# Kernel tuning notes

Measured on AMD Instinct MI355X. Metric: run time of the kernel, lower is better.

Reference implementation:

```python
import jax, jax.numpy as jnp
import numpy as np

BS, NQ, DIM, HEADS, POINTS, LEVELS = 2, 4096, 768, 6, 4, 1
HD = DIM // HEADS
H = W = 64
NV = H * W
EPS = 1e-6


def setup_inputs() -> dict:
    key = jax.random.key(0)
    ks = jax.random.split(key, 16)
    s = 0.02  # param init scale
    return {
        "query": jax.random.normal(ks[0], (BS, NQ, DIM), jnp.float32),
        "reference_points": jax.random.uniform(ks[1], (BS, NQ, LEVELS, 2), jnp.float32),
        "feat": jax.random.normal(ks[2], (BS, NV, DIM), jnp.float32),
        "spatial_shapes": np.array([[H, W]], dtype=np.int64),
        "level_start_index": np.array([0], dtype=np.int64),
        "ln_w": jnp.ones((DIM,), jnp.float32),
        "ln_b": jnp.zeros((DIM,), jnp.float32),
        "vp_w": jax.random.normal(ks[3], (DIM, DIM), jnp.float32) * s,
        "vp_b": jnp.zeros((DIM,), jnp.float32),
        "off_w": jax.random.normal(ks[4], (DIM, HEADS * LEVELS * POINTS * 2), jnp.float32) * s,
        "off_b": jax.random.normal(ks[5], (HEADS * LEVELS * POINTS * 2,), jnp.float32),
        "aw_w": jax.random.normal(ks[6], (DIM, HEADS * LEVELS * POINTS), jnp.float32) * s,
        "aw_b": jnp.zeros((HEADS * LEVELS * POINTS,), jnp.float32),
        "out_w": jax.random.normal(ks[7], (DIM, DIM), jnp.float32) * s,
        "out_b": jnp.zeros((DIM,), jnp.float32),
        "gamma": jax.random.normal(ks[8], (DIM,), jnp.float32) * 0.1,
    }


def _layernorm(x, w, b):
    mu = jnp.mean(x, axis=-1, keepdims=True)
    var = jnp.mean(jnp.square(x - mu), axis=-1, keepdims=True)
    return (x - mu) * jax.lax.rsqrt(var + EPS) * w + b


def _bilinear_sample(img, loc):
    # img: (bs, heads, H, W, hd); loc: (bs, nq, heads, points, 2) in [0,1]
    # matches torch.grid_sample(align_corners=False, padding_mode='zeros')
    bs, heads, h, w, hd = img.shape
    x = loc[..., 0] * w - 0.5
    y = loc[..., 1] * h - 0.5
    x0 = jnp.floor(x)
    y0 = jnp.floor(y)
    wx = x - x0
    wy = y - y0
    x0i = x0.astype(jnp.int32)
    y0i = y0.astype(jnp.int32)
    bi = jnp.arange(bs)[:, None, None, None]
    hi = jnp.arange(heads)[None, None, :, None]

    def gather(yi, xi):
        valid = (xi >= 0) & (xi < w) & (yi >= 0) & (yi < h)
        v = img[bi, hi, jnp.clip(yi, 0, h - 1), jnp.clip(xi, 0, w - 1)]
        return v * valid[..., None].astype(img.dtype)

    v00 = gather(y0i, x0i)
    v01 = gather(y0i, x0i + 1)
    v10 = gather(y0i + 1, x0i)
    v11 = gather(y0i + 1, x0i + 1)
    wx = wx[..., None]
    wy = wy[..., None]
    return (v00 * (1 - wy) * (1 - wx) + v01 * (1 - wy) * wx
            + v10 * wy * (1 - wx) + v11 * wy * wx)


def _msda(q, value, reference_points, spatial_shapes, off_w, off_b, aw_w, aw_b, out_w, out_b):
    bs, nq, _ = q.shape
    nv = value.shape[1]
    value = value.reshape(bs, nv, HEADS, HD)
    offsets = (q @ off_w + off_b).reshape(bs, nq, HEADS, LEVELS, POINTS, 2)
    aw = jax.nn.softmax(q @ aw_w + aw_b, axis=-1).reshape(bs, nq, HEADS, LEVELS, POINTS)
    # offset_normalizer = [W_l, H_l] per level
    norm = jnp.asarray(np.asarray(spatial_shapes)[:, ::-1], jnp.float32)  # (L, 2)
    loc = reference_points[:, :, None, :, None, :] + offsets / norm[None, None, None, :, None, :]
    # loc: (bs, nq, heads, levels, points, 2)
    out = jnp.zeros((bs, nq, HEADS, HD), jnp.float32)
    start = 0
    for l in range(LEVELS):
        h_l, w_l = int(spatial_shapes[l][0]), int(spatial_shapes[l][1])
        img = value[:, start:start + h_l * w_l].reshape(bs, h_l, w_l, HEADS, HD).transpose(0, 3, 1, 2, 4)
        sampled = _bilinear_sample(img, loc[:, :, :, l])  # (bs, nq, heads, points, hd)
        out = out + jnp.einsum('bnhpd,bnhp->bnhd', sampled, aw[:, :, :, l])
        start += h_l * w_l
    return out.reshape(bs, nq, DIM) @ out_w + out_b


def reference(query, reference_points, feat, spatial_shapes, level_start_index,
              ln_w, ln_b, vp_w, vp_b, off_w, off_b, aw_w, aw_b, out_w, out_b, gamma):
    q = _layernorm(query, ln_w, ln_b)
    value = feat @ vp_w + vp_b
    attn = _msda(q, value, reference_points, spatial_shapes,
                 off_w, off_b, aw_w, aw_b, out_w, out_b)
    # identity = zeros, dropout = 0 -> attn as-is; residual scale by gamma
    return query + gamma * attn
```

## Files before the change

### kernel.cpp

```cpp
#include <hip/hip_runtime.h>
#include <hip/hip_bf16.h>
#include <math.h>

#define BSZ 2
#define NQ 4096
#define DIM 768
#define HEADS 6
#define POINTS 4
#define HD 128
#define HW_DIM 64
#define NV (HW_DIM*HW_DIM)
#define M_TOTAL (BSZ*NQ)
#define KDIM 768
#define KSPLIT 4
#define KPART (KDIM/KSPLIT)

#define BM 64
#define BN 128
#define BKK 64
#define NBLK_M (M_TOTAL/BM)
#define NBLK_N (DIM/BN)
#define GEMM_GRID (NBLK_M*NBLK_N)

typedef __attribute__((ext_vector_type(8))) short bf16x8;
typedef __attribute__((ext_vector_type(4))) float f32x4;
typedef unsigned int u32;
typedef unsigned short u16;

__device__ inline u16 f2bf(float f) {
    union { float f; u32 u; } v; v.f = f;
    u32 r = v.u + 0x7fffu + ((v.u >> 16) & 1u);
    return (u16)(r >> 16);
}

#define GLD16(g, l) __builtin_amdgcn_global_load_lds( \
    (const __attribute__((address_space(1))) u32*)(g), \
    (__attribute__((address_space(3))) u32*)(l), 16, 0, 0)

__global__ __launch_bounds__(256) void ln_bf_kernel(const float* __restrict__ x,
        const float* __restrict__ w, const float* __restrict__ b,
        u16* __restrict__ q, const float* __restrict__ feat,
        u16* __restrict__ feat_bf) {
    int row = blockIdx.x;
    int tid = threadIdx.x;
    const float* xr = x + (size_t)row * DIM;
    float v0 = xr[tid], v1 = xr[tid + 256], v2 = xr[tid + 512];
    const float* fr = feat + (size_t)row * DIM;
    u16* fb = feat_bf + (size_t)row * DIM;
    fb[tid]       = f2bf(fr[tid]);
    fb[tid + 256] = f2bf(fr[tid + 256]);
    fb[tid + 512] = f2bf(fr[tid + 512]);

    float s  = v0 + v1 + v2;
    float ss = v0*v0 + v1*v1 + v2*v2;
    __shared__ float red[256], red2[256];
    red[tid] = s; red2[tid] = ss;
    __syncthreads();
    for (int st = 128; st > 0; st >>= 1) {
        if (tid < st) { red[tid] += red[tid + st]; red2[tid] += red2[tid + st]; }
        __syncthreads();
    }
    float mean = red[0] * (1.0f / DIM);
    float var  = red2[0] * (1.0f / DIM) - mean * mean;
    float rstd = rsqrtf(var + 1e-6f);
    u16* qr = q + (size_t)row * DIM;
    qr[tid]       = f2bf((v0 - mean) * rstd * w[tid]       + b[tid]);
    qr[tid + 256] = f2bf((v1 - mean) * rstd * w[tid + 256] + b[tid + 256]);
    qr[tid + 512] = f2bf((v2 - mean) * rstd * w[tid + 512] + b[tid + 512]);
}

__global__ __launch_bounds__(256) void transpose_all(
        const float* __restrict__ vp_w,  u16* __restrict__ vp_wt,
        const float* __restrict__ out_w, u16* __restrict__ out_wt,
        const float* __restrict__ off_w, const float* __restrict__ aw_w,
        u16* __restrict__ oaw_wt) {
    int z = blockIdx.z;
    if (z == 2 && blockIdx.x >= 3) return;
    __shared__ float tile[32][33];
    int n0 = blockIdx.x * 32, k0 = blockIdx.y * 32;
    int tx = threadIdx.x & 31, ty = threadIdx.x >> 5;
    const float* src = (z == 0) ? vp_w : (z == 1) ? out_w : nullptr;
    u16* dst = (z == 0) ? vp_wt : (z == 1) ? out_wt : oaw_wt;
    #pragma unroll
    for (int r = 0; r < 4; r++) {
        int k = k0 + ty + r * 8, n = n0 + tx;
        float v = 0.0f;
        if (z < 2) {
            v = src[(size_t)k * DIM + n];
        } else {
            if (n < 48) v = off_w[(size_t)k * 48 + n];
            else if (n < 72) v = aw_w[(size_t)k * 24 + (n - 48)];
        }
        tile[ty + r * 8][tx] = v;
    }
    __syncthreads();
    #pragma unroll
    for (int r = 0; r < 4; r++) {
        int nn = ty + r * 8, kk = tx;
        int drow = n0 + nn;
        if (z == 2 && drow >= 80) continue;
        dst[(size_t)drow * KDIM + k0 + kk] = f2bf(tile[kk][nn]);
    }
}

__global__ __launch_bounds__(256, 3) void gemm_bt(
        const u16* __restrict__ A, const u16* __restrict__ Bt,
        const float* __restrict__ bias, void* __restrict__ Cout,
        int storeBF16, const float* __restrict__ resid,
        const float* __restrict__ gamma) {
    __shared__ u16 As[BM * BKK];
    __shared__ u16 Bs[BN * BKK];
    int tid = threadIdx.x, w = tid >> 6, lane = tid & 63;
    int lm = lane & 15, quad = lane >> 4;
    int b = blockIdx.x;
    int xcd = b & 7, idx = b >> 3;
    int mb = xcd * 16 + idx / NBLK_N;
    int nb = idx % NBLK_N;
    int m0 = mb * BM, n0 = nb * BN;
    int wr = w & 1, wc = w >> 1;

    int srow = lane >> 3;
    int scol = (lane & 7) ^ srow;
    const u16* Ab = A + (size_t)m0 * KDIM;
    const u16* Bb = Bt + (size_t)n0 * KDIM;

    f32x4 acc[2][4];
    #pragma unroll
    for (int i = 0; i < 2; i++)
        #pragma unroll
        for (int j = 0; j < 4; j++) acc[i][j] = (f32x4){0.f, 0.f, 0.f, 0.f};

    const u16* aaddr[2][2];
    const u16* baddr[4][2];
    #pragma unroll
    for (int i = 0; i < 2; i++) {
        int row = wr * 32 + i * 16 + lm;
        #pragma unroll
        for (int kk = 0; kk < 2; kk++)
            aaddr[i][kk] = &As[row * BKK + (((quad + 4 * kk) ^ (row & 7)) << 3)];
    }
    #pragma unroll
    for (int j = 0; j < 4; j++) {
        int row = wc * 64 + j * 16 + lm;
        #pragma unroll
        for (int kk = 0; kk < 2; kk++)
            baddr[j][kk] = &Bs[row * BKK + (((quad + 4 * kk) ^ (row & 7)) << 3)];
    }

    for (int k0 = 0; k0 < KDIM; k0 += BKK) {
        #pragma unroll
        for (int r = 0; r < 2; r++) {
            int row = r * 32 + w * 8 + srow;
            GLD16(Ab + (size_t)row * KDIM + k0 + scol * 8, &As[(r * 32 + w * 8) * BKK]);
        }
        #pragma unroll
        for (int r = 0; r < 4; r++) {
            int row = r * 32 + w * 8 + srow;
            GLD16(Bb + (size_t)row * KDIM + k0 + scol * 8, &Bs[(r * 32 + w * 8) * BKK]);
        }
        __syncthreads();
        #pragma unroll
        for (int kk = 0; kk < 2; kk++) {
            bf16x8 af[2], bf[4];
            #pragma unroll
            for (int i = 0; i < 2; i++) af[i] = *(const bf16x8*)aaddr[i][kk];
            #pragma unroll
            for (int j = 0; j < 4; j++) bf[j] = *(const bf16x8*)baddr[j][kk];
            #pragma unroll
            for (int i = 0; i < 2; i++)
                #pragma unroll
                for (int j = 0; j < 4; j++)
                    acc[i][j] = __builtin_amdgcn_mfma_f32_16x16x32_bf16(af[i], bf[j], acc[i][j], 0, 0, 0);
        }
        __syncthreads();
    }

    #pragma unroll
    for (int j = 0; j < 4; j++) {
        int col = n0 + wc * 64 + j * 16 + lm;
        float bb = bias[col];
        #pragma unroll
        for (int i = 0; i < 2; i++) {
            #pragma unroll
            for (int r = 0; r < 4; r++) {
                int row = m0 + wr * 32 + i * 16 + quad * 4 + r;
                size_t idxo = (size_t)row * DIM + col;
                float v = acc[i][j][r] + bb;
                if (storeBF16) {
                    ((u16*)Cout)[idxo] = f2bf(v);
                } else {
                    ((float*)Cout)[idxo] = resid[idxo] + gamma[col] * v;
                }
            }
        }
    }
}

__global__ __launch_bounds__(256, 2) void gemm_small(
        const u16* __restrict__ A, const u16* __restrict__ Bt,
        const float* __restrict__ b0, const float* __restrict__ b1,
        float* __restrict__ C, int M, int K) {
    __shared__ u16 As[64 * 32];
    __shared__ u16 Bs[80 * 32];
    int tid = threadIdx.x, wave = tid >> 6, lane = tid & 63;
    int lm = lane & 15, quad = lane >> 4;
    int m0 = blockIdx.x * 64;
    int part = blockIdx.y;
    int kbase = part * KPART;
    f32x4 acc[5];
    #pragma unroll
    for (int i = 0; i < 5; i++) acc[i] = (f32x4){0.f, 0.f, 0.f, 0.f};
    int lrow = lane >> 2, lcol = (lane & 3) * 8;

    for (int k0 = kbase; k0 < kbase + KPART; k0 += 32) {
        for (int c = wave; c < 9; c += 4) {
            if (c < 4) {
                GLD16(A + (size_t)(m0 + c * 16 + lrow) * K + k0 + lcol, &As[c * 16 * 32]);
            } else {
                GLD16(Bt + (size_t)((c - 4) * 16 + lrow) * K + k0 + lcol, &Bs[(c - 4) * 16 * 32]);
            }
        }
        __syncthreads();
        bf16x8 af = *(const bf16x8*)&As[(wave * 16 + lm) * 32 + quad * 8];
        #pragma unroll
        for (int bn = 0; bn < 5; bn++) {
            bf16x8 bv = *(const bf16x8*)&Bs[(bn * 16 + lm) * 32 + quad * 8];
            acc[bn] = __builtin_amdgcn_mfma_f32_16x16x32_bf16(af, bv, acc[bn], 0, 0, 0);
        }
        __syncthreads();
    }
    float* Cp = C + (size_t)part * M_TOTAL * 80;
    #pragma unroll
    for (int bn = 0; bn < 5; bn++) {
        int col = bn * 16 + lm;
        float bb = 0.0f;
        if (part == 0) bb = (col < 48) ? b0[col] : ((col < 72) ? b1[col - 48] : 0.0f);
        #pragma unroll
        for (int r = 0; r < 4; r++) {
            int row = m0 + wave * 16 + quad * 4 + r;
            Cp[(size_t)row * 80 + col] = acc[bn][r] + bb;
        }
    }
}

__global__ __launch_bounds__(384) void sample_kernel(
        const float* __restrict__ oa, const float* __restrict__ refp,
        const u16* __restrict__ v, u16* __restrict__ out) {
    int row = blockIdx.x;
    int b = row >> 12;
    int tid = threadIdx.x;
    __shared__ float s_w[4][24];
    __shared__ int   s_o[4][24];
    __shared__ float s_e[24];
    if (tid < 24) {
        int h = tid >> 2, p = tid & 3;
        float ox = 0.f, oy = 0.f, lg = 0.f;
        #pragma unroll
        for (int part = 0; part < KSPLIT; part++) {
            const float* pp = oa + (size_t)part * M_TOTAL * 80 + (size_t)row * 80;
            ox += pp[h * 8 + p * 2 + 0];
            oy += pp[h * 8 + p * 2 + 1];
            lg += pp[48 + tid];
        }
        float rx = refp[row * 2 + 0], ry = refp[row * 2 + 1];
        float x = (rx + ox * (1.0f / HW_DIM)) * HW_DIM - 0.5f;
        float y = (ry + oy * (1.0f / HW_DIM)) * HW_DIM - 0.5f;
        float fx = floorf(x), fy = floorf(y);
        int x0 = (int)fx, y0 = (int)fy;
        int x1 = x0 + 1, y1 = y0 + 1;
        float wx = x - fx, wy = y - fy;
        float vx0 = (x0 >= 0 && x0 < HW_DIM) ? 1.f : 0.f;
        float vx1 = (x1 >= 0 && x1 < HW_DIM) ? 1.f : 0.f;
        float vy0 = (y0 >= 0 && y0 < HW_DIM) ? 1.f : 0.f;
        float vy1 = (y1 >= 0 && y1 < HW_DIM) ? 1.f : 0.f;
        int xc0 = min(max(x0, 0), HW_DIM - 1), xc1 = min(max(x1, 0), HW_DIM - 1);
        int yc0 = min(max(y0, 0), HW_DIM - 1), yc1 = min(max(y1, 0), HW_DIM - 1);
        int base = b * NV * DIM;
        s_o[0][tid] = base + (yc0 * HW_DIM + xc0) * DIM;
        s_o[1][tid] = base + (yc0 * HW_DIM + xc1) * DIM;
        s_o[2][tid] = base + (yc1 * HW_DIM + xc0) * DIM;
        s_o[3][tid] = base + (yc1 * HW_DIM + xc1) * DIM;
        s_w[0][tid] = (1.f - wy) * (1.f - wx) * vy0 * vx0;
        s_w[1][tid] = (1.f - wy) * wx * vy0 * vx1;
        s_w[2][tid] = wy * (1.f - wx) * vy1 * vx0;
        s_w[3][tid] = wy * wx * vy1 * vx1;
        s_e[tid] = lg;
        float m = s_e[0];
        #pragma unroll
        for (int i = 1; i < 24; i++) m = fmaxf(m, s_e[i]);
        s_e[tid] = expf(lg - m);
    }
    __syncthreads();
    float ssum = 0.0f;
    #pragma unroll
    for (int i = 0; i < 24; i++) ssum += s_e[i];
    float inv = 1.0f / ssum;

    int h = tid >> 6;
    int d2 = (tid & 63) * 2;
    const u16* vb = v + h * HD + d2;
    float a0 = 0.0f, a1 = 0.0f;
    #pragma unroll
    for (int p = 0; p < 4; p++) {
        int idx = h * 4 + p;
        float aw = s_e[idx] * inv;
        #pragma unroll
        for (int c = 0; c < 4; c++) {
            u32 u = *(const u32*)(vb + s_o[c][idx]);
            float w = aw * s_w[c][idx];
            a0 += w * __uint_as_float(u << 16);
            a1 += w * __uint_as_float(u & 0xffff0000u);
        }
    }
    u32 pack = (u32)f2bf(a0) | ((u32)f2bf(a1) << 16);
    *(u32*)&out[(size_t)row * DIM + h * HD + d2] = pack;
}

extern "C" void kernel_launch(void* const* d_in, const int* in_sizes, int n_in,
                              void* d_out, int out_size, void* d_ws, size_t ws_size,
                              hipStream_t stream) {
    const float* query = (const float*)d_in[0];
    const float* refp  = (const float*)d_in[1];
    const float* feat  = (const float*)d_in[2];
    const float* ln_w  = (const float*)d_in[5];
    const float* ln_b  = (const float*)d_in[6];
    const float* vp_w  = (const float*)d_in[7];
    const float* vp_b  = (const float*)d_in[8];
    const float* off_w = (const float*)d_in[9];
    const float* off_b = (const float*)d_in[10];
    const float* aw_w  = (const float*)d_in[11];
    const float* aw_b  = (const float*)d_in[12];
    const float* out_w = (const float*)d_in[13];
    const float* out_b = (const float*)d_in[14];
    const float* gamma = (const float*)d_in[15];

    const size_t MD = (size_t)M_TOTAL * DIM;
    char* ws = (char*)d_ws;
    u16* q_bf    = (u16*)ws;                 ws += MD * 2;
    u16* feat_bf = (u16*)ws;                 ws += MD * 2;
    u16* v_bf    = (u16*)ws;                 ws += MD * 2;
    u16* s_bf    = (u16*)ws;                 ws += MD * 2;
    u16* vp_wt   = (u16*)ws;                 ws += (size_t)DIM * DIM * 2;
    u16* out_wt  = (u16*)ws;                 ws += (size_t)DIM * DIM * 2;
    u16* oaw_wt  = (u16*)ws;                 ws += (size_t)80 * KDIM * 2;
    float* oa    = (float*)ws;               ws += (size_t)KSPLIT * M_TOTAL * 80 * 4;
    float* out_f = (float*)d_out;

    ln_bf_kernel<<<M_TOTAL, 256, 0, stream>>>(query, ln_w, ln_b, q_bf, feat, feat_bf);
    transpose_all<<<dim3(24, 24, 3), 256, 0, stream>>>(vp_w, vp_wt, out_w, out_wt,
                                                       off_w, aw_w, oaw_wt);
    gemm_bt<<<GEMM_GRID, 256, 0, stream>>>(feat_bf, vp_wt, vp_b, v_bf,
                                           1, nullptr, nullptr);
    gemm_small<<<dim3(128, KSPLIT), 256, 0, stream>>>(q_bf, oaw_wt, off_b, aw_b, oa, M_TOTAL, KDIM);
    sample_kernel<<<M_TOTAL, 384, 0, stream>>>(oa, refp, v_bf, s_bf);
    gemm_bt<<<GEMM_GRID, 256, 0, stream>>>(s_bf, out_wt, out_b, out_f,
                                           0, query, gamma);
}
```

Measured before the change: 195.5 us.

## Fuse feat bf16 conversion into value GEMM and use wave-per-row LayerNorm

The value-projection GEMM now loads fp32 feat directly, converts it to bf16 in registers and writes it to swizzled LDS. This removes the separate conversion pass and its bf16 intermediate buffer. LayerNorm is rewritten to give each wave one row, using float4 loads and shuffle reductions instead of an LDS tree with barriers. The tradeoff is that the A-tile load in the fused GEMM becomes synchronous register loads rather than async global-to-LDS copies, and it reads twice as many bytes per tile.

```diff
diff --git a/kernel.cpp b/kernel.cpp
--- a/kernel.cpp
+++ b/kernel.cpp
@@ -39,34 +39,40 @@
 
 __global__ __launch_bounds__(256) void ln_bf_kernel(const float* __restrict__ x,
         const float* __restrict__ w, const float* __restrict__ b,
-        u16* __restrict__ q, const float* __restrict__ feat,
-        u16* __restrict__ feat_bf) {
-    int row = blockIdx.x;
-    int tid = threadIdx.x;
+        u16* __restrict__ q) {
+    int wave = threadIdx.x >> 6, lane = threadIdx.x & 63;
+    int row = blockIdx.x * 4 + wave;
+    int c = lane * 4;
     const float* xr = x + (size_t)row * DIM;
-    float v0 = xr[tid], v1 = xr[tid + 256], v2 = xr[tid + 512];
-    const float* fr = feat + (size_t)row * DIM;
-    u16* fb = feat_bf + (size_t)row * DIM;
-    fb[tid]       = f2bf(fr[tid]);
-    fb[tid + 256] = f2bf(fr[tid + 256]);
-    fb[tid + 512] = f2bf(fr[tid + 512]);
-
-    float s  = v0 + v1 + v2;
-    float ss = v0*v0 + v1*v1 + v2*v2;
-    __shared__ float red[256], red2[256];
-    red[tid] = s; red2[tid] = ss;
-    __syncthreads();
-    for (int st = 128; st > 0; st >>= 1) {
-        if (tid < st) { red[tid] += red[tid + st]; red2[tid] += red2[tid + st]; }
-        __syncthreads();
-    }
-    float mean = red[0] * (1.0f / DIM);
-    float var  = red2[0] * (1.0f / DIM) - mean * mean;
+    float4 v0 = *(const float4*)(xr + c);
+    float4 v1 = *(const float4*)(xr + c + 256);
+    float4 v2 = *(const float4*)(xr + c + 512);
+    float s  = v0.x+v0.y+v0.z+v0.w + v1.x+v1.y+v1.z+v1.w + v2.x+v2.y+v2.z+v2.w;
+    float ss = v0.x*v0.x+v0.y*v0.y+v0.z*v0.z+v0.w*v0.w
+             + v1.x*v1.x+v1.y*v1.y+v1.z*v1.z+v1.w*v1.w
+             + v2.x*v2.x+v2.y*v2.y+v2.z*v2.z+v2.w*v2.w;
+    #pragma unroll
+    for (int st = 1; st < 64; st <<= 1) {
+        s  += __shfl_xor(s,  st, 64);
+        ss += __shfl_xor(ss, st, 64);
+    }
+    float mean = s * (1.0f / DIM);
+    float var  = ss * (1.0f / DIM) - mean * mean;
     float rstd = rsqrtf(var + 1e-6f);
     u16* qr = q + (size_t)row * DIM;
-    qr[tid]       = f2bf((v0 - mean) * rstd * w[tid]       + b[tid]);
-    qr[tid + 256] = f2bf((v1 - mean) * rstd * w[tid + 256] + b[tid + 256]);
-    qr[tid + 512] = f2bf((v2 - mean) * rstd * w[tid + 512] + b[tid + 512]);
+    #pragma unroll
+    for (int g = 0; g < 3; g++) {
+        float4 v = (g == 0) ? v0 : (g == 1) ? v1 : v2;
+        int cc = c + g * 256;
+        const float4 ww = *(const float4*)(w + cc);
+        const float4 bb = *(const float4*)(b + cc);
+        ushort4 o;
+        o.x = f2bf((v.x - mean) * rstd * ww.x + bb.x);
+        o.y = f2bf((v.y - mean) * rstd * ww.y + bb.y);
+        o.z = f2bf((v.z - mean) * rstd * ww.z + bb.z);
+        o.w = f2bf((v.w - mean) * rstd * ww.w + bb.w);
+        *(ushort4*)(qr + cc) = o;
+    }
 }
 
 __global__ __launch_bounds__(256) void transpose_all(
@@ -103,8 +109,9 @@
     }
 }
 
+template<int AFP32>
 __global__ __launch_bounds__(256, 3) void gemm_bt(
-        const u16* __restrict__ A, const u16* __restrict__ Bt,
+        const void* __restrict__ Avoid, const u16* __restrict__ Bt,
         const float* __restrict__ bias, void* __restrict__ Cout,
         int storeBF16, const float* __restrict__ resid,
         const float* __restrict__ gamma) {
@@ -121,8 +128,10 @@
 
     int srow = lane >> 3;
     int scol = (lane & 7) ^ srow;
-    const u16* Ab = A + (size_t)m0 * KDIM;
     const u16* Bb = Bt + (size_t)n0 * KDIM;
+    const u16* Ab16 = (const u16*)Avoid + (size_t)m0 * KDIM;
+    const float* Ab32 = (const float*)Avoid + (size_t)m0 * KDIM;
+    int arow = tid >> 2, acb0 = (tid & 3) * 2;
 
     f32x4 acc[2][4];
     #pragma unroll
@@ -148,10 +157,25 @@
     }
 
     for (int k0 = 0; k0 < KDIM; k0 += BKK) {
-        #pragma unroll
-        for (int r = 0; r < 2; r++) {
-            int row = r * 32 + w * 8 + srow;
-            GLD16(Ab + (size_t)row * KDIM + k0 + scol * 8, &As[(r * 32 + w * 8) * BKK]);
+        if (AFP32) {
+            const float* ag = Ab32 + (size_t)arow * KDIM + k0 + acb0 * 8;
+            float4 f0 = *(const float4*)ag;
+            float4 f1 = *(const float4*)(ag + 4);
+            float4 f2 = *(const float4*)(ag + 8);
+            float4 f3 = *(const float4*)(ag + 12);
+            bf16x8 p0, p1;
+            p0[0]=f2bf(f0.x); p0[1]=f2bf(f0.y); p0[2]=f2bf(f0.z); p0[3]=f2bf(f0.w);
+            p0[4]=f2bf(f1.x); p0[5]=f2bf(f1.y); p0[6]=f2bf(f1.z); p0[7]=f2bf(f1.w);
+            p1[0]=f2bf(f2.x); p1[1]=f2bf(f2.y); p1[2]=f2bf(f2.z); p1[3]=f2bf(f2.w);
+            p1[4]=f2bf(f3.x); p1[5]=f2bf(f3.y); p1[6]=f2bf(f3.z); p1[7]=f2bf(f3.w);
+            *(bf16x8*)&As[arow * BKK + (((acb0)     ^ (arow & 7)) << 3)] = p0;
+            *(bf16x8*)&As[arow * BKK + (((acb0 + 1) ^ (arow & 7)) << 3)] = p1;
+        } else {
+            #pragma unroll
+            for (int r = 0; r < 2; r++) {
+                int row = r * 32 + w * 8 + srow;
+                GLD16(Ab16 + (size_t)row * KDIM + k0 + scol * 8, &As[(r * 32 + w * 8) * BKK]);
+            }
         }
         #pragma unroll
         for (int r = 0; r < 4; r++) {
@@ -337,7 +361,6 @@
     const size_t MD = (size_t)M_TOTAL * DIM;
     char* ws = (char*)d_ws;
     u16* q_bf    = (u16*)ws;                 ws += MD * 2;
-    u16* feat_bf = (u16*)ws;                 ws += MD * 2;
     u16* v_bf    = (u16*)ws;                 ws += MD * 2;
     u16* s_bf    = (u16*)ws;                 ws += MD * 2;
     u16* vp_wt   = (u16*)ws;                 ws += (size_t)DIM * DIM * 2;
@@ -346,13 +369,13 @@
     float* oa    = (float*)ws;               ws += (size_t)KSPLIT * M_TOTAL * 80 * 4;
     float* out_f = (float*)d_out;
 
-    ln_bf_kernel<<<M_TOTAL, 256, 0, stream>>>(query, ln_w, ln_b, q_bf, feat, feat_bf);
+    ln_bf_kernel<<<M_TOTAL / 4, 256, 0, stream>>>(query, ln_w, ln_b, q_bf);
     transpose_all<<<dim3(24, 24, 3), 256, 0, stream>>>(vp_w, vp_wt, out_w, out_wt,
                                                        off_w, aw_w, oaw_wt);
-    gemm_bt<<<GEMM_GRID, 256, 0, stream>>>(feat_bf, vp_wt, vp_b, v_bf,
-                                           1, nullptr, nullptr);
+    gemm_bt<1><<<GEMM_GRID, 256, 0, stream>>>(feat, vp_wt, vp_b, v_bf,
+                                              1, nullptr, nullptr);
     gemm_small<<<dim3(128, KSPLIT), 256, 0, stream>>>(q_bf, oaw_wt, off_b, aw_b, oa, M_TOTAL, KDIM);
     sample_kernel<<<M_TOTAL, 384, 0, stream>>>(oa, refp, v_bf, s_bf);
-    gemm_bt<<<GEMM_GRID, 256, 0, stream>>>(s_bf, out_wt, out_b, out_f,
-                                           0, query, gamma);
-}
+    gemm_bt<0><<<GEMM_GRID, 256, 0, stream>>>(s_bf, out_wt, out_b, out_f,
+                                              0, query, gamma);
+}
```

Measured after the change: 200.7 us. +2.7%, slower.
